# Performance work log

Measured on AMD Instinct MI355X. Metric: run time of the kernel, lower is better.

## Reference

```python
import jax, jax.numpy as jnp
import numpy as np

WIDTH = 32
DEPTH = 3
B, J, K = 16, 256, 384
C_MODEL, C_OBS, C_META = 1, 1, 6
C_IN = C_MODEL + C_OBS + C_META  # concat channels fed to image_mlp


def _mlp(h, W_stack, b_stack):
    # depth x (Linear -> ReLU) hidden blocks
    for d in range(W_stack.shape[0]):
        h = jax.nn.relu(h @ W_stack[d] + b_stack[d])
    return h


def setup_inputs() -> dict:
    key = jax.random.key(0)
    ks = jax.random.split(key, 14)
    Imodel = jax.random.normal(ks[0], (B, J, K, C_MODEL), jnp.float32)
    Iobs = jax.random.normal(ks[1], (B, J, K, C_OBS), jnp.float32)
    metadata = jax.random.normal(ks[2], (B, J, K, C_META), jnp.float32)
    mask = jax.random.randint(ks[3], (B, J, K, 1), 0, 2) > 0

    def init_w(k, fan_in, fan_out):
        return jax.random.normal(k, (fan_in, fan_out), jnp.float32) / np.sqrt(fan_in)

    params = dict(
        W_img_in=init_w(ks[4], C_IN, WIDTH),
        b_img_in=jnp.zeros((WIDTH,), jnp.float32),
        W_img=jax.random.normal(ks[5], (DEPTH, WIDTH, WIDTH), jnp.float32) / np.sqrt(WIDTH),
        b_img=jnp.zeros((DEPTH, WIDTH), jnp.float32),
        W_lin_in=init_w(ks[6], C_META, WIDTH),
        b_lin_in=jnp.zeros((WIDTH,), jnp.float32),
        W_mlp=jax.random.normal(ks[7], (DEPTH, WIDTH, WIDTH), jnp.float32) / np.sqrt(WIDTH),
        b_mlp=jnp.zeros((DEPTH, WIDTH), jnp.float32),
        W_out=init_w(ks[8], WIDTH, 1),
        b_out=jnp.zeros((1,), jnp.float32),
    )
    return dict(Imodel=Imodel, Iobs=Iobs, metadata=metadata, mask=mask,
                sample_size=32, **params)


def reference(Imodel, Iobs, metadata, mask, sample_size,
              W_img_in, b_img_in, W_img, b_img,
              W_lin_in, b_lin_in, W_mlp, b_mlp, W_out, b_out):
    batch = Iobs.shape[0]
    # p: probability of each image having any observed reflection, normalized
    p = jnp.any(mask, axis=-2)[..., 0].astype(jnp.float32)  # [B, J]
    p = p / jnp.sum(p, axis=-1, keepdims=True)
    # multinomial without replacement via Gumbel top-k (fixed key)
    g = jax.random.gumbel(jax.random.key(42), p.shape, jnp.float32)
    scores = jnp.log(p) + g  # -inf where p == 0, never selected
    _, j = jax.lax.top_k(scores, sample_size)  # [B, S]
    idx = j[:, :, None, None]  # broadcast over K and channel dims

    im = jnp.take_along_axis(Imodel, idx, axis=1)    # [B, S, K, 1]
    io = jnp.take_along_axis(Iobs, idx, axis=1)      # [B, S, K, 1]
    md = jnp.take_along_axis(metadata, idx, axis=1)  # [B, S, K, 6]
    image_data = jnp.concatenate((im, io, md), axis=-1)  # [B, S, K, 8]
    image_mask = jnp.take_along_axis(mask, idx, axis=1).astype(jnp.float32)  # [B, S, K, 1]

    # image_mlp: input linear + depth hidden blocks
    h = image_data @ W_img_in + b_img_in
    h = _mlp(h, W_img, b_img)  # [B, S, K, WIDTH]
    # masked mean over sampled reflections
    image_rep = jnp.sum(image_mask * h, axis=(1, 2), keepdims=True)
    image_rep = image_rep / jnp.sum(image_mask, axis=(1, 2), keepdims=True)  # [B,1,1,WIDTH]

    scale = metadata @ W_lin_in + b_lin_in  # [B, J, K, WIDTH]
    scale = scale + image_rep
    scale = _mlp(scale, W_mlp, b_mlp)
    scale = scale @ W_out + b_out  # [B, J, K, 1]
    return jnp.where(mask, scale, 0.0)
```

## Files before the change

kernel.cpp:

```cpp
#include <hip/hip_runtime.h>
#include <hip/hip_bf16.h>
#include <stdint.h>

#define BB   16
#define JJ   256
#define KK   384
#define NROW (BB * JJ)
#define NPOS ((size_t)BB * JJ * KK)

#define WS_FLAG  0
#define WS_SEL   64
#define WS_VINT  2176
#define WS_VBYTE (WS_VINT + NROW * 4)
#define WS_PART  (WS_VBYTE + NROW * 4)
#define WS_REPB  (WS_PART + 512 * 33 * 4)

typedef float f32x4 __attribute__((ext_vector_type(4)));
typedef short bf16x8 __attribute__((ext_vector_type(8)));

struct FragU { union { bf16x8 v; uint32_t u[4]; }; };

#define PIN(x) asm volatile("" : "+v"(x))

__device__ __forceinline__ uint32_t rotl32(uint32_t x, int r) {
  return (x << r) | (x >> (32 - r));
}

__device__ __forceinline__ void threefry2x32_k42(uint32_t c0, uint32_t c1,
                                                 uint32_t& o0, uint32_t& o1) {
  const uint32_t ks0 = 0u, ks1 = 42u, ks2 = 0x1BD11BDAu ^ 0u ^ 42u;
  uint32_t x0 = c0 + ks0, x1 = c1 + ks1;
#define TFR(r) { x0 += x1; x1 = rotl32(x1, r); x1 ^= x0; }
  TFR(13) TFR(15) TFR(26) TFR(6)   x0 += ks1; x1 += ks2 + 1u;
  TFR(17) TFR(29) TFR(16) TFR(24)  x0 += ks2; x1 += ks0 + 2u;
  TFR(13) TFR(15) TFR(26) TFR(6)   x0 += ks0; x1 += ks1 + 3u;
  TFR(17) TFR(29) TFR(16) TFR(24)  x0 += ks1; x1 += ks2 + 4u;
  TFR(13) TFR(15) TFR(26) TFR(6)   x0 += ks2; x1 += ks0 + 5u;
#undef TFR
  o0 = x0; o1 = x1;
}

__device__ __forceinline__ uint32_t jax_bits(uint32_t t) {
  uint32_t o0, o1;
  threefry2x32_k42(0u, t, o0, o1);
  return o0 ^ o1;
}

__device__ __forceinline__ void split2(float x, short& h, short& l) {
  const unsigned short hu = __builtin_bit_cast(unsigned short, __float2bfloat16(x));
  const float hf = __builtin_bit_cast(float, (uint32_t)hu << 16);
  h = (short)hu;
  l = (short)__builtin_bit_cast(unsigned short, __float2bfloat16(x - hf));
}

__device__ __forceinline__ void split_pk(float x0, float x1,
                                         uint32_t& ph, uint32_t& pl) {
  const uint32_t h0 = (uint32_t)__builtin_bit_cast(unsigned short, __float2bfloat16(x0));
  const uint32_t h1 = (uint32_t)__builtin_bit_cast(unsigned short, __float2bfloat16(x1));
  ph = h0 | (h1 << 16);
  const float f0 = __builtin_bit_cast(float, h0 << 16);
  const float f1 = __builtin_bit_cast(float, h1 << 16);
  const uint32_t l0 = (uint32_t)__builtin_bit_cast(unsigned short, __float2bfloat16(x0 - f0));
  const uint32_t l1 = (uint32_t)__builtin_bit_cast(unsigned short, __float2bfloat16(x1 - f1));
  pl = l0 | (l1 << 16);
}

__device__ __forceinline__ void refrag_ll(const f32x4 dT0, const f32x4 dT1,
                                          bf16x8& Bh, bf16x8& Bl) {
  FragU H, L;
  split_pk(dT0[0], dT0[1], H.u[0], L.u[0]);
  split_pk(dT0[2], dT0[3], H.u[1], L.u[1]);
  split_pk(dT1[0], dT1[1], H.u[2], L.u[2]);
  split_pk(dT1[2], dT1[3], H.u[3], L.u[3]);
  Bh = H.v; Bl = L.v;
}

__device__ __forceinline__ void refrag_br(f32x4 dT0, f32x4 dT1,
                                          const f32x4 b0, const f32x4 b1,
                                          bf16x8& Bh, bf16x8& Bl) {
#pragma unroll
  for (int r = 0; r < 4; ++r) {
    dT0[r] = fmaxf(dT0[r] + b0[r], 0.f);
    dT1[r] = fmaxf(dT1[r] + b1[r], 0.f);
  }
  refrag_ll(dT0, dT1, Bh, Bl);
}

__global__ __launch_bounds__(256) void k_valid(const void* __restrict__ maskp,
                                               int* __restrict__ valid_int,
                                               int* __restrict__ valid_byte) {
  const int row = blockIdx.x * 4 + (threadIdx.x >> 6);
  const int lane = threadIdx.x & 63;
  const uint32_t* wi = (const uint32_t*)maskp + (size_t)row * 384;
  int v = 0;
#pragma unroll
  for (int i = 0; i < 6; ++i) v |= (wi[lane + i * 64] != 0u);
  const unsigned long long bi = __ballot(v);
  const uint32_t* wb = (const uint32_t*)maskp + (size_t)row * 96;
  int u = 0;
  for (int i = lane; i < 96; i += 64) u |= (wb[i] != 0u);
  const unsigned long long bu = __ballot(u);
  if (lane == 0) {
    valid_int[row] = (bi != 0ull) ? 1 : 0;
    valid_byte[row] = (bu != 0ull) ? 1 : 0;
  }
}

__global__ void k_select(const void* __restrict__ maskp,
                         const int* __restrict__ valid_int,
                         const int* __restrict__ valid_byte,
                         const int* __restrict__ sample_size,
                         int* __restrict__ flag_out, int* __restrict__ sel) {
  const int b = blockIdx.x, lane = threadIdx.x;
  const uint32_t* mw = (const uint32_t*)maskp;
  int big = 0;
#pragma unroll
  for (int i = 0; i < 16; ++i) big |= (mw[lane + i * 64] > 1u);
  const int fl = (__ballot(big) != 0ull) ? 1 : 0;
  if (b == 0 && lane == 0) flag_out[0] = fl;
  const int* valid = fl ? valid_byte : valid_int;

  uint32_t comp[4];
#pragma unroll
  for (int q = 0; q < 4; ++q) {
    const int j = lane * 4 + q;
    const uint32_t ub = jax_bits((uint32_t)(b * 256 + j)) >> 9;
    const uint32_t key = valid[b * 256 + j] ? (ub + 1u) : 0u;
    comp[q] = (key << 8) | (uint32_t)(255 - j);
  }
  int S = sample_size[0];
  if (S > 32) S = 32;
  for (int s = 0; s < S; ++s) {
    uint32_t wm = comp[0];
    wm = comp[1] > wm ? comp[1] : wm;
    wm = comp[2] > wm ? comp[2] : wm;
    wm = comp[3] > wm ? comp[3] : wm;
#pragma unroll
    for (int off = 32; off; off >>= 1) {
      const uint32_t o = __shfl_xor(wm, off);
      wm = o > wm ? o : wm;
    }
    if (wm == 0u) {
      if (lane == 0) sel[b * 32 + s] = 0;
    } else {
#pragma unroll
      for (int q = 0; q < 4; ++q) {
        if (comp[q] == wm) {
          sel[b * 32 + s] = 255 - (int)(comp[q] & 0xFFu);
          comp[q] = 0u;
        }
      }
    }
  }
  for (int s2 = S + lane; s2 < 32; s2 += 64) sel[b * 32 + s2] = 0;
}

__global__ __launch_bounds__(256, 1) void k_image(
    const float* __restrict__ Imodel, const float* __restrict__ Iobs,
    const float* __restrict__ md, const void* __restrict__ maskp,
    const int* __restrict__ flag, const int* __restrict__ sel,
    const int* __restrict__ sample_size,
    const float* __restrict__ W_in, const float* __restrict__ b_in,
    const float* __restrict__ Wd, const float* __restrict__ bd,
    float* __restrict__ partial) {
  __shared__ float red[4 * 33];
  const int tid = threadIdx.x, wid = tid >> 6, lane = tid & 63;
  const int g = lane >> 4, c = lane & 15;
  const int blk = blockIdx.x;
  const int b = blk >> 5, s = blk & 31;
  const bool active = (s < sample_size[0]);
  const int j = sel[b * 32 + s] & 255;
  const size_t pos0 = ((size_t)(b * JJ + j)) * KK + (size_t)wid * 96;
  const int fl = flag[0];

  bf16x8 AWi[2];
#pragma unroll
  for (int ct = 0; ct < 2; ++ct) {
    short bh, bl; split2(b_in[ct * 16 + c], bh, bl);
#pragma unroll
    for (int e = 0; e < 8; ++e) {
      short v;
      if (g <= 1) {
        short hh, ll; split2(W_in[e * 32 + ct * 16 + c], hh, ll);
        v = hh;
      } else if (g == 2) {
        short hh, ll; split2(W_in[e * 32 + ct * 16 + c], hh, ll);
        v = ll;
      } else {
        v = (e == 0) ? bh : ((e == 1) ? bl : (short)0);
      }
      AWi[ct][e] = v;
    }
  }

  bf16x8 AhW[3][2], AlW[3][2];
#pragma unroll
  for (int d = 0; d < 3; ++d)
#pragma unroll
    for (int ct = 0; ct < 2; ++ct)
#pragma unroll
      for (int e = 0; e < 8; ++e) {
        const int f = (e < 4) ? (4 * g + e) : (16 + 4 * g + (e - 4));
        short hh, ll; split2(Wd[d * 1024 + f * 32 + ct * 16 + c], hh, ll);
        AhW[d][ct][e] = hh; AlW[d][ct][e] = ll;
      }
  f32x4 bsA[3], bsB[3];
#pragma unroll
  for (int d = 0; d < 3; ++d)
#pragma unroll
    for (int r = 0; r < 4; ++r) {
      bsA[d][r] = bd[d * 32 + 4 * g + r];
      bsB[d][r] = bd[d * 32 + 16 + 4 * g + r];
    }

  f32x4 acc0 = {0.f, 0.f, 0.f, 0.f}, acc1 = {0.f, 0.f, 0.f, 0.f};
  float cntv = 0.f;
  const f32x4 z = {0.f, 0.f, 0.f, 0.f};

  for (int t = 0; t < 6; ++t) {
    PIN(AWi[0]); PIN(AWi[1]);
#pragma unroll
    for (int d = 0; d < 3; ++d) {
      PIN(AhW[d][0]); PIN(AhW[d][1]); PIN(AlW[d][0]); PIN(AlW[d][1]);
    }
    const size_t tb = pos0 + (size_t)t * 16;
    const size_t p = tb + c;
    const float i0 = Imodel[p];
    const float i1 = Iobs[p];
    const float* mp = md + p * 6;
    const float2 v0 = *(const float2*)(mp);
    const float2 v1 = *(const float2*)(mp + 2);
    const float2 v2 = *(const float2*)(mp + 4);
    float m;
    if (fl) m = (((const uint8_t*)maskp)[p] != 0) ? 1.f : 0.f;
    else    m = (((const int*)maskp)[p] != 0) ? 1.f : 0.f;
    if (!active) m = 0.f;

    uint32_t ph[4], pl[4];
    split_pk(i0, i1, ph[0], pl[0]);
    split_pk(v0.x, v0.y, ph[1], pl[1]);
    split_pk(v1.x, v1.y, ph[2], pl[2]);
    split_pk(v2.x, v2.y, ph[3], pl[3]);
    FragU Bi;
#pragma unroll
    for (int i = 0; i < 4; ++i) {
      const uint32_t t0 = (g == 1) ? pl[i] : ph[i];
      Bi.u[i] = (g == 3) ? ((i == 0) ? 0x3F803F80u : 0u) : t0;
    }

    f32x4 dT0 = __builtin_amdgcn_mfma_f32_16x16x32_bf16(AWi[0], Bi.v, z, 0, 0, 0);
    f32x4 dT1 = __builtin_amdgcn_mfma_f32_16x16x32_bf16(AWi[1], Bi.v, z, 0, 0, 0);
    bf16x8 Bh, Bl;
    refrag_ll(dT0, dT1, Bh, Bl);

#pragma unroll
    for (int d = 0; d < 3; ++d) {
      dT0 = __builtin_amdgcn_mfma_f32_16x16x32_bf16(AhW[d][0], Bh, z, 0, 0, 0);
      dT1 = __builtin_amdgcn_mfma_f32_16x16x32_bf16(AhW[d][1], Bh, z, 0, 0, 0);
      dT0 = __builtin_amdgcn_mfma_f32_16x16x32_bf16(AlW[d][0], Bh, dT0, 0, 0, 0);
      dT1 = __builtin_amdgcn_mfma_f32_16x16x32_bf16(AlW[d][1], Bh, dT1, 0, 0, 0);
      dT0 = __builtin_amdgcn_mfma_f32_16x16x32_bf16(AhW[d][0], Bl, dT0, 0, 0, 0);
      dT1 = __builtin_amdgcn_mfma_f32_16x16x32_bf16(AhW[d][1], Bl, dT1, 0, 0, 0);
      if (d < 2) {
        refrag_br(dT0, dT1, bsA[d], bsB[d], Bh, Bl);
      } else {
#pragma unroll
        for (int r = 0; r < 4; ++r) {
          acc0[r] = fmaf(m, fmaxf(dT0[r] + bsA[2][r], 0.f), acc0[r]);
          acc1[r] = fmaf(m, fmaxf(dT1[r] + bsB[2][r], 0.f), acc1[r]);
        }
        cntv += m;
      }
    }
  }

#pragma unroll
  for (int off = 1; off < 16; off <<= 1) {
#pragma unroll
    for (int r = 0; r < 4; ++r) {
      acc0[r] += __shfl_xor(acc0[r], off);
      acc1[r] += __shfl_xor(acc1[r], off);
    }
    cntv += __shfl_xor(cntv, off);
  }
  if (c == 0) {
#pragma unroll
    for (int r = 0; r < 4; ++r) {
      red[wid * 33 + 4 * g + r] = acc0[r];
      red[wid * 33 + 16 + 4 * g + r] = acc1[r];
    }
    if (g == 0) red[wid * 33 + 32] = cntv;
  }
  __syncthreads();
  if (tid < 33) {
    partial[blk * 33 + tid] =
        red[tid] + red[33 + tid] + red[66 + tid] + red[99 + tid];
  }
}

__global__ void k_rep(const float* __restrict__ partial,
                      const float* __restrict__ b_lin,
                      float* __restrict__ rep_bias) {
  const int b = blockIdx.x, n = threadIdx.x;
  float sum = 0.f, cnt = 0.f;
  for (int s = 0; s < 32; ++s) {
    sum += partial[(b * 32 + s) * 33 + n];
    cnt += partial[(b * 32 + s) * 33 + 32];
  }
  rep_bias[b * 32 + n] = b_lin[n] + sum / cnt;
}

__global__ __launch_bounds__(256, 1) void k_scale(
    const float* __restrict__ md, const void* __restrict__ maskp,
    const int* __restrict__ flag,
    const float* __restrict__ W_lin, const float* __restrict__ rep_bias,
    const float* __restrict__ Wd, const float* __restrict__ bd,
    const float* __restrict__ W_out, const float* __restrict__ b_out,
    float* __restrict__ out) {
  const int tid = threadIdx.x;
  const int wid = tid >> 6, lane = tid & 63;
  const int g = lane >> 4, c = lane & 15;
  const int job = blockIdx.x * 4 + wid;
  const int b = job / 384;
  const size_t pos0 = (size_t)job * 256;
  const int fl = flag[0];
  const bool gLt2 = (g < 2);

  bf16x8 AW[2];
#pragma unroll
  for (int ct = 0; ct < 2; ++ct) {
    short rbh, rbl; split2(rep_bias[b * 32 + ct * 16 + c], rbh, rbl);
#pragma unroll
    for (int e = 0; e < 8; ++e) {
      short v = 0;
      if (e < 6) {
        short wh, wl; split2(W_lin[e * 32 + ct * 16 + c], wh, wl);
        v = gLt2 ? wh : wl;
      } else if (g == 0) {
        v = (e == 6) ? rbh : rbl;
      }
      AW[ct][e] = v;
    }
  }

  bf16x8 AhW[3][2], AlW[3][2];
#pragma unroll
  for (int d = 0; d < 3; ++d)
#pragma unroll
    for (int ct = 0; ct < 2; ++ct)
#pragma unroll
      for (int e = 0; e < 8; ++e) {
        const int f = (e < 4) ? (4 * g + e) : (16 + 4 * g + (e - 4));
        short hh, ll; split2(Wd[d * 1024 + f * 32 + ct * 16 + c], hh, ll);
        AhW[d][ct][e] = hh; AlW[d][ct][e] = ll;
      }
  f32x4 bsA[3], bsB[3];
#pragma unroll
  for (int d = 0; d < 3; ++d)
#pragma unroll
    for (int r = 0; r < 4; ++r) {
      bsA[d][r] = bd[d * 32 + 4 * g + r];
      bsB[d][r] = bd[d * 32 + 16 + 4 * g + r];
    }
  f32x4 woA, woB;
#pragma unroll
  for (int r = 0; r < 4; ++r) {
    woA[r] = W_out[4 * g + r];
    woB[r] = W_out[16 + 4 * g + r];
  }
  const float bo = b_out[0];
  const uint32_t bias_word = (g == 0) ? 0x00003F80u : 0u;

  float mvA[6], mvB[6];
  uint32_t mkA, mkB;
  {
    const float* ra = md + (pos0 + c) * 6;
    const float2 a01 = *(const float2*)(ra);
    const float2 a23 = *(const float2*)(ra + 2);
    const float2 a45 = *(const float2*)(ra + 4);
    mvA[0] = a01.x; mvA[1] = a01.y; mvA[2] = a23.x;
    mvA[3] = a23.y; mvA[4] = a45.x; mvA[5] = a45.y;
    const float* rb2 = md + (pos0 + 16 + c) * 6;
    const float2 b01 = *(const float2*)(rb2);
    const float2 b23 = *(const float2*)(rb2 + 2);
    const float2 b45 = *(const float2*)(rb2 + 4);
    mvB[0] = b01.x; mvB[1] = b01.y; mvB[2] = b23.x;
    mvB[3] = b23.y; mvB[4] = b45.x; mvB[5] = b45.y;
    if (fl) {
      mkA = (uint32_t)((const uint8_t*)maskp)[pos0 + c];
      mkB = (uint32_t)((const uint8_t*)maskp)[pos0 + 16 + c];
    } else {
      mkA = ((const uint32_t*)maskp)[pos0 + c];
      mkB = ((const uint32_t*)maskp)[pos0 + 16 + c];
    }
  }

  const f32x4 z = {0.f, 0.f, 0.f, 0.f};

  for (int tp = 0; tp < 8; ++tp) {
    PIN(AW[0]); PIN(AW[1]);
#pragma unroll
    for (int d = 0; d < 3; ++d) {
      PIN(AhW[d][0]); PIN(AhW[d][1]); PIN(AlW[d][0]); PIN(AlW[d][1]);
      PIN(bsA[d]); PIN(bsB[d]);
    }
    PIN(woA); PIN(woB);

    const size_t tbA = pos0 + (size_t)tp * 32;
    const size_t tbB = tbA + 16;

    float nvA[6] = {0, 0, 0, 0, 0, 0}, nvB[6] = {0, 0, 0, 0, 0, 0};
    uint32_t nkA = 0, nkB = 0;
    if (tp < 7) {
      const float* ra = md + (tbA + 32 + c) * 6;
      const float2 a01 = *(const float2*)(ra);
      const float2 a23 = *(const float2*)(ra + 2);
      const float2 a45 = *(const float2*)(ra + 4);
      nvA[0] = a01.x; nvA[1] = a01.y; nvA[2] = a23.x;
      nvA[3] = a23.y; nvA[4] = a45.x; nvA[5] = a45.y;
      const float* rb2 = md + (tbA + 48 + c) * 6;
      const float2 b01 = *(const float2*)(rb2);
      const float2 b23 = *(const float2*)(rb2 + 2);
      const float2 b45 = *(const float2*)(rb2 + 4);
      nvB[0] = b01.x; nvB[1] = b01.y; nvB[2] = b23.x;
      nvB[3] = b23.y; nvB[4] = b45.x; nvB[5] = b45.y;
      if (fl) {
        nkA = (uint32_t)((const uint8_t*)maskp)[tbA + 32 + c];
        nkB = (uint32_t)((const uint8_t*)maskp)[tbA + 48 + c];
      } else {
        nkA = ((const uint32_t*)maskp)[tbA + 32 + c];
        nkB = ((const uint32_t*)maskp)[tbA + 48 + c];
      }
    }

    FragU BinA, BinB;
    {
      uint32_t ph0, pl0, ph1, pl1, ph2, pl2;
      split_pk(mvA[0], mvA[1], ph0, pl0);
      split_pk(mvA[2], mvA[3], ph1, pl1);
      split_pk(mvA[4], mvA[5], ph2, pl2);
      BinA.u[0] = (g & 1) ? pl0 : ph0;
      BinA.u[1] = (g & 1) ? pl1 : ph1;
      BinA.u[2] = (g & 1) ? pl2 : ph2;
      BinA.u[3] = bias_word;
      split_pk(mvB[0], mvB[1], ph0, pl0);
      split_pk(mvB[2], mvB[3], ph1, pl1);
      split_pk(mvB[4], mvB[5], ph2, pl2);
      BinB.u[0] = (g & 1) ? pl0 : ph0;
      BinB.u[1] = (g & 1) ? pl1 : ph1;
      BinB.u[2] = (g & 1) ? pl2 : ph2;
      BinB.u[3] = bias_word;
    }

    f32x4 dT0A = __builtin_amdgcn_mfma_f32_16x16x32_bf16(AW[0], BinA.v, z, 0, 0, 0);
    f32x4 dT0B = __builtin_amdgcn_mfma_f32_16x16x32_bf16(AW[0], BinB.v, z, 0, 0, 0);
    f32x4 dT1A = __builtin_amdgcn_mfma_f32_16x16x32_bf16(AW[1], BinA.v, z, 0, 0, 0);
    f32x4 dT1B = __builtin_amdgcn_mfma_f32_16x16x32_bf16(AW[1], BinB.v, z, 0, 0, 0);

    bf16x8 BhA, BlA, BhB, BlB;
    refrag_ll(dT0A, dT1A, BhA, BlA);
    refrag_ll(dT0B, dT1B, BhB, BlB);

#pragma unroll
    for (int d = 0; d < 3; ++d) {
      dT0A = __builtin_amdgcn_mfma_f32_16x16x32_bf16(AhW[d][0], BhA, z, 0, 0, 0);
      dT0B = __builtin_amdgcn_mfma_f32_16x16x32_bf16(AhW[d][0], BhB, z, 0, 0, 0);
      dT1A = __builtin_amdgcn_mfma_f32_16x16x32_bf16(AhW[d][1], BhA, z, 0, 0, 0);
      dT1B = __builtin_amdgcn_mfma_f32_16x16x32_bf16(AhW[d][1], BhB, z, 0, 0, 0);
      dT0A = __builtin_amdgcn_mfma_f32_16x16x32_bf16(AlW[d][0], BhA, dT0A, 0, 0, 0);
      dT0B = __builtin_amdgcn_mfma_f32_16x16x32_bf16(AlW[d][0], BhB, dT0B, 0, 0, 0);
      dT1A = __builtin_amdgcn_mfma_f32_16x16x32_bf16(AlW[d][1], BhA, dT1A, 0, 0, 0);
      dT1B = __builtin_amdgcn_mfma_f32_16x16x32_bf16(AlW[d][1], BhB, dT1B, 0, 0, 0);
      dT0A = __builtin_amdgcn_mfma_f32_16x16x32_bf16(AhW[d][0], BlA, dT0A, 0, 0, 0);
      dT0B = __builtin_amdgcn_mfma_f32_16x16x32_bf16(AhW[d][0], BlB, dT0B, 0, 0, 0);
      dT1A = __builtin_amdgcn_mfma_f32_16x16x32_bf16(AhW[d][1], BlA, dT1A, 0, 0, 0);
      dT1B = __builtin_amdgcn_mfma_f32_16x16x32_bf16(AhW[d][1], BlB, dT1B, 0, 0, 0);
      if (d < 2) {
        refrag_br(dT0A, dT1A, bsA[d], bsB[d], BhA, BlA);
        refrag_br(dT0B, dT1B, bsA[d], bsB[d], BhB, BlB);
      } else {
        float sumA = 0.f, sumB = 0.f;
#pragma unroll
        for (int r = 0; r < 4; ++r) {
          sumA = fmaf(fmaxf(dT0A[r] + bsA[2][r], 0.f), woA[r], sumA);
          sumA = fmaf(fmaxf(dT1A[r] + bsB[2][r], 0.f), woB[r], sumA);
          sumB = fmaf(fmaxf(dT0B[r] + bsA[2][r], 0.f), woA[r], sumB);
          sumB = fmaf(fmaxf(dT1B[r] + bsB[2][r], 0.f), woB[r], sumB);
        }
        sumA += __shfl_xor(sumA, 16);
        sumA += __shfl_xor(sumA, 32);
        sumB += __shfl_xor(sumB, 16);
        sumB += __shfl_xor(sumB, 32);
        if (g == 0) {
          out[tbA + c] = mkA ? (sumA + bo) : 0.0f;
          out[tbB + c] = mkB ? (sumB + bo) : 0.0f;
        }
      }
    }

#pragma unroll
    for (int i = 0; i < 6; ++i) { mvA[i] = nvA[i]; mvB[i] = nvB[i]; }
    mkA = nkA; mkB = nkB;
  }
}

extern "C" void kernel_launch(void* const* d_in, const int* in_sizes, int n_in,
                              void* d_out, int out_size, void* d_ws, size_t ws_size,
                              hipStream_t stream) {
  const float* Imodel   = (const float*)d_in[0];
  const float* Iobs     = (const float*)d_in[1];
  const float* metadata = (const float*)d_in[2];
  const void*  mask     = d_in[3];
  const int*   sample_size = (const int*)d_in[4];
  const float* W_img_in = (const float*)d_in[5];
  const float* b_img_in = (const float*)d_in[6];
  const float* W_img    = (const float*)d_in[7];
  const float* b_img    = (const float*)d_in[8];
  const float* W_lin_in = (const float*)d_in[9];
  const float* b_lin_in = (const float*)d_in[10];
  const float* W_mlp    = (const float*)d_in[11];
  const float* b_mlp    = (const float*)d_in[12];
  const float* W_out    = (const float*)d_in[13];
  const float* b_out    = (const float*)d_in[14];
  float* out = (float*)d_out;

  char* ws = (char*)d_ws;
  int*   flag     = (int*)(ws + WS_FLAG);
  int*   sel      = (int*)(ws + WS_SEL);
  int*   vint     = (int*)(ws + WS_VINT);
  int*   vbyte    = (int*)(ws + WS_VBYTE);
  float* partial  = (float*)(ws + WS_PART);
  float* rep_bias = (float*)(ws + WS_REPB);

  k_valid<<<NROW / 4, 256, 0, stream>>>(mask, vint, vbyte);
  k_select<<<BB, 64, 0, stream>>>(mask, vint, vbyte, sample_size, flag, sel);
  k_image<<<512, 256, 0, stream>>>(Imodel, Iobs, metadata, mask, flag, sel,
                                   sample_size, W_img_in, b_img_in, W_img,
                                   b_img, partial);
  k_rep<<<BB, 32, 0, stream>>>(partial, b_lin_in, rep_bias);
  k_scale<<<1536, 256, 0, stream>>>(metadata, mask, flag, W_lin_in, rep_bias,
                                    W_mlp, b_mlp, W_out, b_out, out);
}
```

Before: 94.76 us.

## Restructure image MLP: FP32 input layer, activations as A operand, LDS transpose

The k_image kernel now computes the 8-to-32 input layer in FP32 FMAs instead of an MFMA with packed bias tricks. It swaps the MFMA operand roles so activations are the A fragment and weights the B fragment, and re-fragments hidden activations through a per-wave LDS transpose instead of register shuffles. The mask is loaded vectorized per row group, and the final reduction needs fewer shuffles. k_scale drops the PIN register-pinning asm and raises its launch bound to 3 blocks per CU to allow more occupancy, at the risk of register spills.

```diff
diff --git a/kernel.cpp b/kernel.cpp
--- a/kernel.cpp
+++ b/kernel.cpp
@@ -19,8 +19,6 @@
 typedef short bf16x8 __attribute__((ext_vector_type(8)));
 
 struct FragU { union { bf16x8 v; uint32_t u[4]; }; };
-
-#define PIN(x) asm volatile("" : "+v"(x))
 
 __device__ __forceinline__ uint32_t rotl32(uint32_t x, int r) {
   return (x << r) | (x >> (32 - r));
@@ -163,6 +161,7 @@
     const float* __restrict__ W_in, const float* __restrict__ b_in,
     const float* __restrict__ Wd, const float* __restrict__ bd,
     float* __restrict__ partial) {
+  __shared__ float lds_t[4][16 * 36];
   __shared__ float red[4 * 33];
   const int tid = threadIdx.x, wid = tid >> 6, lane = tid & 63;
   const int g = lane >> 4, c = lane & 15;
@@ -173,124 +172,119 @@
   const size_t pos0 = ((size_t)(b * JJ + j)) * KK + (size_t)wid * 96;
   const int fl = flag[0];
 
-  bf16x8 AWi[2];
-#pragma unroll
-  for (int ct = 0; ct < 2; ++ct) {
-    short bh, bl; split2(b_in[ct * 16 + c], bh, bl);
-#pragma unroll
-    for (int e = 0; e < 8; ++e) {
-      short v;
-      if (g <= 1) {
-        short hh, ll; split2(W_in[e * 32 + ct * 16 + c], hh, ll);
-        v = hh;
-      } else if (g == 2) {
-        short hh, ll; split2(W_in[e * 32 + ct * 16 + c], hh, ll);
-        v = ll;
-      } else {
-        v = (e == 0) ? bh : ((e == 1) ? bl : (short)0);
-      }
-      AWi[ct][e] = v;
-    }
-  }
-
-  bf16x8 AhW[3][2], AlW[3][2];
+  float Win[8][8];
+#pragma unroll
+  for (int cc = 0; cc < 8; ++cc)
+#pragma unroll
+    for (int e = 0; e < 8; ++e) Win[cc][e] = W_in[cc * 32 + g * 8 + e];
+  float b0v[8];
+#pragma unroll
+  for (int e = 0; e < 8; ++e) b0v[e] = b_in[g * 8 + e];
+
+  bf16x8 Bh[3][2], Bl[3][2];
 #pragma unroll
   for (int d = 0; d < 3; ++d)
 #pragma unroll
     for (int ct = 0; ct < 2; ++ct)
 #pragma unroll
       for (int e = 0; e < 8; ++e) {
-        const int f = (e < 4) ? (4 * g + e) : (16 + 4 * g + (e - 4));
-        short hh, ll; split2(Wd[d * 1024 + f * 32 + ct * 16 + c], hh, ll);
-        AhW[d][ct][e] = hh; AlW[d][ct][e] = ll;
-      }
-  f32x4 bsA[3], bsB[3];
-#pragma unroll
-  for (int d = 0; d < 3; ++d)
-#pragma unroll
-    for (int r = 0; r < 4; ++r) {
-      bsA[d][r] = bd[d * 32 + 4 * g + r];
-      bsB[d][r] = bd[d * 32 + 16 + 4 * g + r];
-    }
-
-  f32x4 acc0 = {0.f, 0.f, 0.f, 0.f}, acc1 = {0.f, 0.f, 0.f, 0.f};
-  float cntv = 0.f;
-  const f32x4 z = {0.f, 0.f, 0.f, 0.f};
+        const float w = Wd[d * 1024 + (g * 8 + e) * 32 + ct * 16 + c];
+        short hh, ll; split2(w, hh, ll);
+        Bh[d][ct][e] = hh; Bl[d][ct][e] = ll;
+      }
+  float bias_v[3][2];
+#pragma unroll
+  for (int d = 0; d < 3; ++d) {
+    bias_v[d][0] = bd[d * 32 + c];
+    bias_v[d][1] = bd[d * 32 + 16 + c];
+  }
+  float* myl = lds_t[wid];
+
+  float acc0 = 0.f, acc1 = 0.f, cntv = 0.f;
 
   for (int t = 0; t < 6; ++t) {
-    PIN(AWi[0]); PIN(AWi[1]);
-#pragma unroll
-    for (int d = 0; d < 3; ++d) {
-      PIN(AhW[d][0]); PIN(AhW[d][1]); PIN(AlW[d][0]); PIN(AlW[d][1]);
-    }
     const size_t tb = pos0 + (size_t)t * 16;
     const size_t p = tb + c;
-    const float i0 = Imodel[p];
-    const float i1 = Iobs[p];
+    float in[8];
+    in[0] = Imodel[p];
+    in[1] = Iobs[p];
     const float* mp = md + p * 6;
     const float2 v0 = *(const float2*)(mp);
     const float2 v1 = *(const float2*)(mp + 2);
     const float2 v2 = *(const float2*)(mp + 4);
-    float m;
-    if (fl) m = (((const uint8_t*)maskp)[p] != 0) ? 1.f : 0.f;
-    else    m = (((const int*)maskp)[p] != 0) ? 1.f : 0.f;
-    if (!active) m = 0.f;
-
-    uint32_t ph[4], pl[4];
-    split_pk(i0, i1, ph[0], pl[0]);
-    split_pk(v0.x, v0.y, ph[1], pl[1]);
-    split_pk(v1.x, v1.y, ph[2], pl[2]);
-    split_pk(v2.x, v2.y, ph[3], pl[3]);
-    FragU Bi;
-#pragma unroll
-    for (int i = 0; i < 4; ++i) {
-      const uint32_t t0 = (g == 1) ? pl[i] : ph[i];
-      Bi.u[i] = (g == 3) ? ((i == 0) ? 0x3F803F80u : 0u) : t0;
-    }
-
-    f32x4 dT0 = __builtin_amdgcn_mfma_f32_16x16x32_bf16(AWi[0], Bi.v, z, 0, 0, 0);
-    f32x4 dT1 = __builtin_amdgcn_mfma_f32_16x16x32_bf16(AWi[1], Bi.v, z, 0, 0, 0);
-    bf16x8 Bh, Bl;
-    refrag_ll(dT0, dT1, Bh, Bl);
+    in[2] = v0.x; in[3] = v0.y; in[4] = v1.x; in[5] = v1.y;
+    in[6] = v2.x; in[7] = v2.y;
+
+    bf16x8 ah, al;
+#pragma unroll
+    for (int e = 0; e < 8; ++e) {
+      float h = b0v[e];
+#pragma unroll
+      for (int cc = 0; cc < 8; ++cc) h = fmaf(in[cc], Win[cc][e], h);
+      short hh, ll; split2(h, hh, ll);
+      ah[e] = hh; al[e] = ll;
+    }
 
 #pragma unroll
     for (int d = 0; d < 3; ++d) {
-      dT0 = __builtin_amdgcn_mfma_f32_16x16x32_bf16(AhW[d][0], Bh, z, 0, 0, 0);
-      dT1 = __builtin_amdgcn_mfma_f32_16x16x32_bf16(AhW[d][1], Bh, z, 0, 0, 0);
-      dT0 = __builtin_amdgcn_mfma_f32_16x16x32_bf16(AlW[d][0], Bh, dT0, 0, 0, 0);
-      dT1 = __builtin_amdgcn_mfma_f32_16x16x32_bf16(AlW[d][1], Bh, dT1, 0, 0, 0);
-      dT0 = __builtin_amdgcn_mfma_f32_16x16x32_bf16(AhW[d][0], Bl, dT0, 0, 0, 0);
-      dT1 = __builtin_amdgcn_mfma_f32_16x16x32_bf16(AhW[d][1], Bl, dT1, 0, 0, 0);
+      f32x4 a0 = {0.f, 0.f, 0.f, 0.f}, a1 = {0.f, 0.f, 0.f, 0.f};
+      a0 = __builtin_amdgcn_mfma_f32_16x16x32_bf16(ah, Bh[d][0], a0, 0, 0, 0);
+      a0 = __builtin_amdgcn_mfma_f32_16x16x32_bf16(al, Bh[d][0], a0, 0, 0, 0);
+      a0 = __builtin_amdgcn_mfma_f32_16x16x32_bf16(ah, Bl[d][0], a0, 0, 0, 0);
+      a1 = __builtin_amdgcn_mfma_f32_16x16x32_bf16(ah, Bh[d][1], a1, 0, 0, 0);
+      a1 = __builtin_amdgcn_mfma_f32_16x16x32_bf16(al, Bh[d][1], a1, 0, 0, 0);
+      a1 = __builtin_amdgcn_mfma_f32_16x16x32_bf16(ah, Bl[d][1], a1, 0, 0, 0);
+#pragma unroll
+      for (int r = 0; r < 4; ++r) {
+        a0[r] = fmaxf(a0[r] + bias_v[d][0], 0.f);
+        a1[r] = fmaxf(a1[r] + bias_v[d][1], 0.f);
+      }
       if (d < 2) {
-        refrag_br(dT0, dT1, bsA[d], bsB[d], Bh, Bl);
+#pragma unroll
+        for (int r = 0; r < 4; ++r) {
+          myl[(g * 4 + r) * 36 + c] = a0[r];
+          myl[(g * 4 + r) * 36 + 16 + c] = a1[r];
+        }
+#pragma unroll
+        for (int e = 0; e < 8; ++e) {
+          const float h = myl[c * 36 + g * 8 + e];
+          short hh, ll; split2(h, hh, ll);
+          ah[e] = hh; al[e] = ll;
+        }
       } else {
+        float mr[4];
+        if (fl) {
+          const uint32_t mw = *(const uint32_t*)((const uint8_t*)maskp + tb + g * 4);
+          mr[0] = (mw & 0x000000FFu) ? 1.f : 0.f;
+          mr[1] = (mw & 0x0000FF00u) ? 1.f : 0.f;
+          mr[2] = (mw & 0x00FF0000u) ? 1.f : 0.f;
+          mr[3] = (mw & 0xFF000000u) ? 1.f : 0.f;
+        } else {
+          const int4 mi = *(const int4*)((const int*)maskp + tb + g * 4);
+          mr[0] = mi.x ? 1.f : 0.f;
+          mr[1] = mi.y ? 1.f : 0.f;
+          mr[2] = mi.z ? 1.f : 0.f;
+          mr[3] = mi.w ? 1.f : 0.f;
+        }
+        if (!active) { mr[0] = mr[1] = mr[2] = mr[3] = 0.f; }
 #pragma unroll
         for (int r = 0; r < 4; ++r) {
-          acc0[r] = fmaf(m, fmaxf(dT0[r] + bsA[2][r], 0.f), acc0[r]);
-          acc1[r] = fmaf(m, fmaxf(dT1[r] + bsB[2][r], 0.f), acc1[r]);
-        }
-        cntv += m;
-      }
-    }
-  }
-
-#pragma unroll
-  for (int off = 1; off < 16; off <<= 1) {
-#pragma unroll
-    for (int r = 0; r < 4; ++r) {
-      acc0[r] += __shfl_xor(acc0[r], off);
-      acc1[r] += __shfl_xor(acc1[r], off);
-    }
-    cntv += __shfl_xor(cntv, off);
-  }
-  if (c == 0) {
-#pragma unroll
-    for (int r = 0; r < 4; ++r) {
-      red[wid * 33 + 4 * g + r] = acc0[r];
-      red[wid * 33 + 16 + 4 * g + r] = acc1[r];
-    }
-    if (g == 0) red[wid * 33 + 32] = cntv;
-  }
+          acc0 = fmaf(mr[r], a0[r], acc0);
+          acc1 = fmaf(mr[r], a1[r], acc1);
+          cntv += mr[r];
+        }
+      }
+    }
+  }
+
+  acc0 += __shfl_xor(acc0, 16); acc0 += __shfl_xor(acc0, 32);
+  acc1 += __shfl_xor(acc1, 16); acc1 += __shfl_xor(acc1, 32);
+  cntv += __shfl_xor(cntv, 16); cntv += __shfl_xor(cntv, 32);
+  if (lane < 16) {
+    red[wid * 33 + lane] = acc0;
+    red[wid * 33 + 16 + lane] = acc1;
+  }
+  if (lane == 0) red[wid * 33 + 32] = cntv;
   __syncthreads();
   if (tid < 33) {
     partial[blk * 33 + tid] =
@@ -310,7 +304,7 @@
   rep_bias[b * 32 + n] = b_lin[n] + sum / cnt;
 }
 
-__global__ __launch_bounds__(256, 1) void k_scale(
+__global__ __launch_bounds__(256, 3) void k_scale(
     const float* __restrict__ md, const void* __restrict__ maskp,
     const int* __restrict__ flag,
     const float* __restrict__ W_lin, const float* __restrict__ rep_bias,
@@ -329,7 +323,8 @@
   bf16x8 AW[2];
 #pragma unroll
   for (int ct = 0; ct < 2; ++ct) {
-    short rbh, rbl; split2(rep_bias[b * 32 + ct * 16 + c], rbh, rbl);
+    const float rb = rep_bias[b * 32 + ct * 16 + c];
+    short rbh, rbl; split2(rb, rbh, rbl);
 #pragma unroll
     for (int e = 0; e < 8; ++e) {
       short v = 0;
@@ -398,14 +393,6 @@
   const f32x4 z = {0.f, 0.f, 0.f, 0.f};
 
   for (int tp = 0; tp < 8; ++tp) {
-    PIN(AW[0]); PIN(AW[1]);
-#pragma unroll
-    for (int d = 0; d < 3; ++d) {
-      PIN(AhW[d][0]); PIN(AhW[d][1]); PIN(AlW[d][0]); PIN(AlW[d][1]);
-      PIN(bsA[d]); PIN(bsB[d]);
-    }
-    PIN(woA); PIN(woB);
-
     const size_t tbA = pos0 + (size_t)tp * 32;
     const size_t tbB = tbA + 16;
 
```

New measurement: 85.69 us. 9.6% less time.

## Simplify scale loop, raise occupancy, use packed bf16 split conversions

Applied to the files above, without the earlier changes.

Rewrites the k_scale main loop to handle one 16-position tile per iteration with compiler unrolling, replacing the manual two-tile interleave and software prefetch. It drops the PIN register pinning and raises launch bounds to 3 blocks per CU, relying on occupancy rather than explicit ILP to hide latency. split_pk now takes the high bf16 half by truncation with a byte perm and packs the low half with v_cvt_pk_bf16_f32. Truncating the high half changes rounding of the hi/lo split slightly, and fewer registers per thread could cause spills or less overlap.

```diff
diff --git a/kernel.cpp b/kernel.cpp
--- a/kernel.cpp
+++ b/kernel.cpp
@@ -19,8 +19,6 @@
 typedef short bf16x8 __attribute__((ext_vector_type(8)));
 
 struct FragU { union { bf16x8 v; uint32_t u[4]; }; };
-
-#define PIN(x) asm volatile("" : "+v"(x))
 
 __device__ __forceinline__ uint32_t rotl32(uint32_t x, int r) {
   return (x << r) | (x >> (32 - r));
@@ -55,14 +53,14 @@
 
 __device__ __forceinline__ void split_pk(float x0, float x1,
                                          uint32_t& ph, uint32_t& pl) {
-  const uint32_t h0 = (uint32_t)__builtin_bit_cast(unsigned short, __float2bfloat16(x0));
-  const uint32_t h1 = (uint32_t)__builtin_bit_cast(unsigned short, __float2bfloat16(x1));
-  ph = h0 | (h1 << 16);
-  const float f0 = __builtin_bit_cast(float, h0 << 16);
-  const float f1 = __builtin_bit_cast(float, h1 << 16);
-  const uint32_t l0 = (uint32_t)__builtin_bit_cast(unsigned short, __float2bfloat16(x0 - f0));
-  const uint32_t l1 = (uint32_t)__builtin_bit_cast(unsigned short, __float2bfloat16(x1 - f1));
-  pl = l0 | (l1 << 16);
+  const uint32_t u0 = __builtin_bit_cast(uint32_t, x0);
+  const uint32_t u1 = __builtin_bit_cast(uint32_t, x1);
+  ph = __builtin_amdgcn_perm(u1, u0, 0x07060302u);
+  const float r0 = x0 - __builtin_bit_cast(float, u0 & 0xFFFF0000u);
+  const float r1 = x1 - __builtin_bit_cast(float, u1 & 0xFFFF0000u);
+  uint32_t p;
+  asm("v_cvt_pk_bf16_f32 %0, %1, %2" : "=v"(p) : "v"(r0), "v"(r1));
+  pl = p;
 }
 
 __device__ __forceinline__ void refrag_ll(const f32x4 dT0, const f32x4 dT1,
@@ -217,12 +215,8 @@
   float cntv = 0.f;
   const f32x4 z = {0.f, 0.f, 0.f, 0.f};
 
+#pragma unroll 2
   for (int t = 0; t < 6; ++t) {
-    PIN(AWi[0]); PIN(AWi[1]);
-#pragma unroll
-    for (int d = 0; d < 3; ++d) {
-      PIN(AhW[d][0]); PIN(AhW[d][1]); PIN(AlW[d][0]); PIN(AlW[d][1]);
-    }
     const size_t tb = pos0 + (size_t)t * 16;
     const size_t p = tb + c;
     const float i0 = Imodel[p];
@@ -310,7 +304,7 @@
   rep_bias[b * 32 + n] = b_lin[n] + sum / cnt;
 }
 
-__global__ __launch_bounds__(256, 1) void k_scale(
+__global__ __launch_bounds__(256, 3) void k_scale(
     const float* __restrict__ md, const void* __restrict__ maskp,
     const int* __restrict__ flag,
     const float* __restrict__ W_lin, const float* __restrict__ rep_bias,
@@ -329,7 +323,8 @@
   bf16x8 AW[2];
 #pragma unroll
   for (int ct = 0; ct < 2; ++ct) {
-    short rbh, rbl; split2(rep_bias[b * 32 + ct * 16 + c], rbh, rbl);
+    const float rb = rep_bias[b * 32 + ct * 16 + c];
+    short rbh, rbl; split2(rb, rbh, rbl);
 #pragma unroll
     for (int e = 0; e < 8; ++e) {
       short v = 0;
@@ -370,137 +365,64 @@
   }
   const float bo = b_out[0];
   const uint32_t bias_word = (g == 0) ? 0x00003F80u : 0u;
-
-  float mvA[6], mvB[6];
-  uint32_t mkA, mkB;
-  {
-    const float* ra = md + (pos0 + c) * 6;
-    const float2 a01 = *(const float2*)(ra);
-    const float2 a23 = *(const float2*)(ra + 2);
-    const float2 a45 = *(const float2*)(ra + 4);
-    mvA[0] = a01.x; mvA[1] = a01.y; mvA[2] = a23.x;
-    mvA[3] = a23.y; mvA[4] = a45.x; mvA[5] = a45.y;
-    const float* rb2 = md + (pos0 + 16 + c) * 6;
-    const float2 b01 = *(const float2*)(rb2);
-    const float2 b23 = *(const float2*)(rb2 + 2);
-    const float2 b45 = *(const float2*)(rb2 + 4);
-    mvB[0] = b01.x; mvB[1] = b01.y; mvB[2] = b23.x;
-    mvB[3] = b23.y; mvB[4] = b45.x; mvB[5] = b45.y;
-    if (fl) {
-      mkA = (uint32_t)((const uint8_t*)maskp)[pos0 + c];
-      mkB = (uint32_t)((const uint8_t*)maskp)[pos0 + 16 + c];
-    } else {
-      mkA = ((const uint32_t*)maskp)[pos0 + c];
-      mkB = ((const uint32_t*)maskp)[pos0 + 16 + c];
-    }
-  }
-
   const f32x4 z = {0.f, 0.f, 0.f, 0.f};
 
-  for (int tp = 0; tp < 8; ++tp) {
-    PIN(AW[0]); PIN(AW[1]);
-#pragma unroll
-    for (int d = 0; d < 3; ++d) {
-      PIN(AhW[d][0]); PIN(AhW[d][1]); PIN(AlW[d][0]); PIN(AlW[d][1]);
-      PIN(bsA[d]); PIN(bsB[d]);
-    }
-    PIN(woA); PIN(woB);
-
-    const size_t tbA = pos0 + (size_t)tp * 32;
-    const size_t tbB = tbA + 16;
-
-    float nvA[6] = {0, 0, 0, 0, 0, 0}, nvB[6] = {0, 0, 0, 0, 0, 0};
-    uint32_t nkA = 0, nkB = 0;
-    if (tp < 7) {
-      const float* ra = md + (tbA + 32 + c) * 6;
-      const float2 a01 = *(const float2*)(ra);
-      const float2 a23 = *(const float2*)(ra + 2);
-      const float2 a45 = *(const float2*)(ra + 4);
-      nvA[0] = a01.x; nvA[1] = a01.y; nvA[2] = a23.x;
-      nvA[3] = a23.y; nvA[4] = a45.x; nvA[5] = a45.y;
-      const float* rb2 = md + (tbA + 48 + c) * 6;
-      const float2 b01 = *(const float2*)(rb2);
-      const float2 b23 = *(const float2*)(rb2 + 2);
-      const float2 b45 = *(const float2*)(rb2 + 4);
-      nvB[0] = b01.x; nvB[1] = b01.y; nvB[2] = b23.x;
-      nvB[3] = b23.y; nvB[4] = b45.x; nvB[5] = b45.y;
-      if (fl) {
-        nkA = (uint32_t)((const uint8_t*)maskp)[tbA + 32 + c];
-        nkB = (uint32_t)((const uint8_t*)maskp)[tbA + 48 + c];
-      } else {
-        nkA = ((const uint32_t*)maskp)[tbA + 32 + c];
-        nkB = ((const uint32_t*)maskp)[tbA + 48 + c];
-      }
-    }
-
-    FragU BinA, BinB;
+  const float* mdp = md + (pos0 + c) * 6;
+  const uint8_t* mb8 = (const uint8_t*)maskp + pos0 + c;
+  const uint32_t* mb32 = (const uint32_t*)maskp + pos0 + c;
+
+#pragma unroll 4
+  for (int t = 0; t < 16; ++t) {
+    const size_t tb = pos0 + (size_t)t * 16;
+
+    const float* mrow = mdp + t * 96;
+    const float2 a01 = *(const float2*)(mrow);
+    const float2 a23 = *(const float2*)(mrow + 2);
+    const float2 a45 = *(const float2*)(mrow + 4);
+    uint32_t mk;
+    if (fl) mk = (uint32_t)mb8[t * 16];
+    else    mk = mb32[t * 16];
+
+    FragU Bin;
     {
       uint32_t ph0, pl0, ph1, pl1, ph2, pl2;
-      split_pk(mvA[0], mvA[1], ph0, pl0);
-      split_pk(mvA[2], mvA[3], ph1, pl1);
-      split_pk(mvA[4], mvA[5], ph2, pl2);
-      BinA.u[0] = (g & 1) ? pl0 : ph0;
-      BinA.u[1] = (g & 1) ? pl1 : ph1;
-      BinA.u[2] = (g & 1) ? pl2 : ph2;
-      BinA.u[3] = bias_word;
-      split_pk(mvB[0], mvB[1], ph0, pl0);
-      split_pk(mvB[2], mvB[3], ph1, pl1);
-      split_pk(mvB[4], mvB[5], ph2, pl2);
-      BinB.u[0] = (g & 1) ? pl0 : ph0;
-      BinB.u[1] = (g & 1) ? pl1 : ph1;
-      BinB.u[2] = (g & 1) ? pl2 : ph2;
-      BinB.u[3] = bias_word;
-    }
-
-    f32x4 dT0A = __builtin_amdgcn_mfma_f32_16x16x32_bf16(AW[0], BinA.v, z, 0, 0, 0);
-    f32x4 dT0B = __builtin_amdgcn_mfma_f32_16x16x32_bf16(AW[0], BinB.v, z, 0, 0, 0);
-    f32x4 dT1A = __builtin_amdgcn_mfma_f32_16x16x32_bf16(AW[1], BinA.v, z, 0, 0, 0);
-    f32x4 dT1B = __builtin_amdgcn_mfma_f32_16x16x32_bf16(AW[1], BinB.v, z, 0, 0, 0);
-
-    bf16x8 BhA, BlA, BhB, BlB;
-    refrag_ll(dT0A, dT1A, BhA, BlA);
-    refrag_ll(dT0B, dT1B, BhB, BlB);
+      split_pk(a01.x, a01.y, ph0, pl0);
+      split_pk(a23.x, a23.y, ph1, pl1);
+      split_pk(a45.x, a45.y, ph2, pl2);
+      Bin.u[0] = (g & 1) ? pl0 : ph0;
+      Bin.u[1] = (g & 1) ? pl1 : ph1;
+      Bin.u[2] = (g & 1) ? pl2 : ph2;
+      Bin.u[3] = bias_word;
+    }
+
+    f32x4 dT0 = __builtin_amdgcn_mfma_f32_16x16x32_bf16(AW[0], Bin.v, z, 0, 0, 0);
+    f32x4 dT1 = __builtin_amdgcn_mfma_f32_16x16x32_bf16(AW[1], Bin.v, z, 0, 0, 0);
+
+    bf16x8 Bh, Bl;
+    refrag_ll(dT0, dT1, Bh, Bl);
 
 #pragma unroll
     for (int d = 0; d < 3; ++d) {
-      dT0A = __builtin_amdgcn_mfma_f32_16x16x32_bf16(AhW[d][0], BhA, z, 0, 0, 0);
-      dT0B = __builtin_amdgcn_mfma_f32_16x16x32_bf16(AhW[d][0], BhB, z, 0, 0, 0);
-      dT1A = __builtin_amdgcn_mfma_f32_16x16x32_bf16(AhW[d][1], BhA, z, 0, 0, 0);
-      dT1B = __builtin_amdgcn_mfma_f32_16x16x32_bf16(AhW[d][1], BhB, z, 0, 0, 0);
-      dT0A = __builtin_amdgcn_mfma_f32_16x16x32_bf16(AlW[d][0], BhA, dT0A, 0, 0, 0);
-      dT0B = __builtin_amdgcn_mfma_f32_16x16x32_bf16(AlW[d][0], BhB, dT0B, 0, 0, 0);
-      dT1A = __builtin_amdgcn_mfma_f32_16x16x32_bf16(AlW[d][1], BhA, dT1A, 0, 0, 0);
-      dT1B = __builtin_amdgcn_mfma_f32_16x16x32_bf16(AlW[d][1], BhB, dT1B, 0, 0, 0);
-      dT0A = __builtin_amdgcn_mfma_f32_16x16x32_bf16(AhW[d][0], BlA, dT0A, 0, 0, 0);
-      dT0B = __builtin_amdgcn_mfma_f32_16x16x32_bf16(AhW[d][0], BlB, dT0B, 0, 0, 0);
-      dT1A = __builtin_amdgcn_mfma_f32_16x16x32_bf16(AhW[d][1], BlA, dT1A, 0, 0, 0);
-      dT1B = __builtin_amdgcn_mfma_f32_16x16x32_bf16(AhW[d][1], BlB, dT1B, 0, 0, 0);
+      dT0 = __builtin_amdgcn_mfma_f32_16x16x32_bf16(AhW[d][0], Bh, z, 0, 0, 0);
+      dT1 = __builtin_amdgcn_mfma_f32_16x16x32_bf16(AhW[d][1], Bh, z, 0, 0, 0);
+      dT0 = __builtin_amdgcn_mfma_f32_16x16x32_bf16(AlW[d][0], Bh, dT0, 0, 0, 0);
+      dT1 = __builtin_amdgcn_mfma_f32_16x16x32_bf16(AlW[d][1], Bh, dT1, 0, 0, 0);
+      dT0 = __builtin_amdgcn_mfma_f32_16x16x32_bf16(AhW[d][0], Bl, dT0, 0, 0, 0);
+      dT1 = __builtin_amdgcn_mfma_f32_16x16x32_bf16(AhW[d][1], Bl, dT1, 0, 0, 0);
       if (d < 2) {
-        refrag_br(dT0A, dT1A, bsA[d], bsB[d], BhA, BlA);
-        refrag_br(dT0B, dT1B, bsA[d], bsB[d], BhB, BlB);
+        refrag_br(dT0, dT1, bsA[d], bsB[d], Bh, Bl);
       } else {
-        float sumA = 0.f, sumB = 0.f;
+        float sum = 0.f;
 #pragma unroll
         for (int r = 0; r < 4; ++r) {
-          sumA = fmaf(fmaxf(dT0A[r] + bsA[2][r], 0.f), woA[r], sumA);
-          sumA = fmaf(fmaxf(dT1A[r] + bsB[2][r], 0.f), woB[r], sumA);
-          sumB = fmaf(fmaxf(dT0B[r] + bsA[2][r], 0.f), woA[r], sumB);
-          sumB = fmaf(fmaxf(dT1B[r] + bsB[2][r], 0.f), woB[r], sumB);
+          sum = fmaf(fmaxf(dT0[r] + bsA[2][r], 0.f), woA[r], sum);
+          sum = fmaf(fmaxf(dT1[r] + bsB[2][r], 0.f), woB[r], sum);
         }
-        sumA += __shfl_xor(sumA, 16);
-        sumA += __shfl_xor(sumA, 32);
-        sumB += __shfl_xor(sumB, 16);
-        sumB += __shfl_xor(sumB, 32);
-        if (g == 0) {
-          out[tbA + c] = mkA ? (sumA + bo) : 0.0f;
-          out[tbB + c] = mkB ? (sumB + bo) : 0.0f;
-        }
-      }
-    }
-
-#pragma unroll
-    for (int i = 0; i < 6; ++i) { mvA[i] = nvA[i]; mvB[i] = nvB[i]; }
-    mkA = nkA; mkB = nkB;
+        sum += __shfl_xor(sum, 16);
+        sum += __shfl_xor(sum, 32);
+        if (g == 0) out[tb + c] = mk ? (sum + bo) : 0.0f;
+      }
+    }
   }
 }
 
```

After: 82.99 us. 12.4% less time.
